# Performance work log

Hardware: AMD Instinct MI355X
Metric: run time of the kernel (lower is better)

## Reference

```python
import jax, jax.numpy as jnp
import numpy as np

B, T, D = 2, 4096, 1024
H, L = 8, 2
DH = D // H           # 128
BS = 64               # bucket_size (lucidrains default)
NH = 8                # n_hashes (lucidrains default)
NB = T // BS          # 64 buckets (even, required)
FF = 4 * D


def setup_inputs() -> dict:
    key = jax.random.key(0)
    ks = jax.random.split(key, 16)
    s = 0.02
    return {
        'x': jax.random.normal(ks[0], (B, T, D), jnp.float32),
        'Wqk': jax.random.normal(ks[1], (L, D, H * DH), jnp.float32) * s,
        'Wv': jax.random.normal(ks[2], (L, D, H * DH), jnp.float32) * s,
        'Wout': jax.random.normal(ks[3], (L, H * DH, D), jnp.float32) * s,
        'bout': jnp.zeros((L, D), jnp.float32),
        'ln1_g': jnp.ones((L, D), jnp.float32),
        'ln1_b': jnp.zeros((L, D), jnp.float32),
        'W1': jax.random.normal(ks[4], (L, D, FF), jnp.float32) * s,
        'b1': jnp.zeros((L, FF), jnp.float32),
        'W2': jax.random.normal(ks[5], (L, FF, D), jnp.float32) * s,
        'b2': jnp.zeros((L, D), jnp.float32),
        'ln2_g': jnp.ones((L, D), jnp.float32),
        'ln2_b': jnp.zeros((L, D), jnp.float32),
        'rotations': jax.random.normal(ks[6], (L, DH, NH, NB // 2), jnp.float32),
    }


def _layer_norm(x, g, b):
    m = jnp.mean(x, axis=-1, keepdims=True)
    v = jnp.var(x, axis=-1, keepdims=True)
    return (x - m) * jax.lax.rsqrt(v + 1e-5) * g + b


def _look_one_back(x):
    # concat each chunk with the previous chunk (wrap-around), along the within-chunk axis
    return jnp.concatenate([x, jnp.roll(x, 1, axis=1)], axis=2)


def _lsh_attention(qk, v, rot):
    # qk, v: (bh, T, DH); rot: (DH, NH, NB//2). Causal LSH attention (lucidrains defaults).
    bh, t, d = qk.shape
    rotated = jnp.einsum('btd,dhr->bhtr', qk, rot)
    rotated = jnp.concatenate([rotated, -rotated], axis=-1)          # (bh, NH, T, NB)
    buckets = jnp.argmax(rotated, axis=-1)                            # (bh, NH, T)
    buckets = buckets + (jnp.arange(NH) * NB)[None, :, None]
    buckets = buckets.reshape(bh, NH * t)
    ticker = jnp.arange(NH * t)
    buckets_and_t = buckets * t + (ticker % t)
    sticker = jnp.argsort(buckets_and_t, axis=-1)                     # stable
    undo_sort = jnp.argsort(sticker, axis=-1)
    st = sticker % t                                                  # original positions
    sqk = jnp.take_along_axis(qk, st[..., None], axis=1)              # (bh, NH*T, DH)
    sv = jnp.take_along_axis(v, st[..., None], axis=1)
    n_chunks = NH * NB
    bq = sqk.reshape(bh, n_chunks, BS, d)
    norm = jnp.maximum(jnp.linalg.norm(sqk, axis=-1, keepdims=True), 1e-12)
    bk = (sqk / norm).reshape(bh, n_chunks, BS, d)
    bv = sv.reshape(bh, n_chunks, BS, d)
    bk = _look_one_back(bk)                                           # (bh, nc, 2*BS, d)
    bv = _look_one_back(bv)
    dots = jnp.einsum('bcie,bcje->bcij', bq, bk) * (d ** -0.5)
    bq_t = st.reshape(bh, n_chunks, BS)
    bkv_t = _look_one_back(bq_t[..., None] * jnp.ones((1,), st.dtype))[..., 0] if False else jnp.concatenate([bq_t, jnp.roll(bq_t, 1, axis=1)], axis=2)
    causal = bq_t[:, :, :, None] < bkv_t[:, :, None, :]
    dots = jnp.where(causal, -1e9, dots)
    self_mask = bq_t[:, :, :, None] == bkv_t[:, :, None, :]
    dots = jnp.where(self_mask, -5e4, dots)                           # TOKEN_SELF_ATTN_VALUE
    lse = jax.scipy.special.logsumexp(dots, axis=-1, keepdims=True)
    p = jnp.exp(dots - lse)
    bo = jnp.einsum('bcij,bcje->bcie', p, bv)
    so = bo.reshape(bh, NH * t, d)
    o = jnp.take_along_axis(so, undo_sort[..., None], axis=1)
    logits = jnp.take_along_axis(lse.reshape(bh, NH * t), undo_sort, axis=1)
    o = o.reshape(bh, NH, t, d)
    logits = logits.reshape(bh, NH, t, 1)
    probs = jnp.exp(logits - jax.scipy.special.logsumexp(logits, axis=1, keepdims=True))
    return jnp.sum(o * probs, axis=1)                                 # (bh, T, DH)


def _attn_block(x, Wqk, Wv, Wout, bout, g, b, rot):
    h = _layer_norm(x, g, b)
    qk = (h @ Wqk).reshape(B, T, H, DH).transpose(0, 2, 1, 3).reshape(B * H, T, DH)
    v = (h @ Wv).reshape(B, T, H, DH).transpose(0, 2, 1, 3).reshape(B * H, T, DH)
    o = _lsh_attention(qk, v, rot)
    o = o.reshape(B, H, T, DH).transpose(0, 2, 1, 3).reshape(B, T, H * DH)
    return o @ Wout + bout


def _ff_block(x, W1, b1, W2, b2, g, b):
    h = _layer_norm(x, g, b)
    return jax.nn.gelu(h @ W1 + b1, approximate=False) @ W2 + b2


def reference(x, Wqk, Wv, Wout, bout, ln1_g, ln1_b, W1, b1, W2, b2, ln2_g, ln2_b, rotations):
    # Reversible Reformer: x duplicated into two streams
    x1, x2 = x, x
    for l in range(L):
        x1 = x1 + _attn_block(x2, Wqk[l], Wv[l], Wout[l], bout[l], ln1_g[l], ln1_b[l], rotations[l])
        x2 = x2 + _ff_block(x1, W1[l], b1[l], W2[l], b2[l], ln2_g[l], ln2_b[l])
    out = (x1 + x2) * 0.5
    # mean-pool over sequence, reshape (1, B, D)
    return jnp.mean(out, axis=1).reshape(1, -1, D)
```

## Files before the change

### kernel.cpp

```cpp
#include <hip/hip_runtime.h>
#include <hip/hip_bf16.h>
#include <stdint.h>

#define B_ 2
#define T_ 4096
#define D_ 1024
#define H_ 8
#define DH_ 128
#define L_ 2
#define BS_ 64
#define NH_ 8
#define NB_ 64
#define NC_ (NH_*NB_)
#define FF_ 4096
#define BH_ (B_*H_)

typedef __hip_bfloat16 bf16;
typedef __attribute__((ext_vector_type(8))) short short8;
typedef __attribute__((ext_vector_type(4))) float f32x4;

typedef __attribute__((address_space(3))) uint32_t lds_u32_t;
typedef const __attribute__((address_space(1))) uint32_t glb_u32_t;

__device__ __forceinline__ void async_load16(const void* g, void* l) {
  __builtin_amdgcn_global_load_lds((glb_u32_t*)g, (lds_u32_t*)l, 16, 0, 0);
}

__global__ void diag_kernel(float* __restrict__ out, float a, float b) {
  if (threadIdx.x == 0) { out[0] = a; out[1] = b; }
}

__global__ void copy2_kernel(const float* __restrict__ x, float* __restrict__ x1,
                             float* __restrict__ x2) {
  int idx = blockIdx.x * 256 + threadIdx.x;
  if (idx < B_ * T_ * D_ / 4) {
    float4 v = ((const float4*)x)[idx];
    ((float4*)x1)[idx] = v;
    ((float4*)x2)[idx] = v;
  }
}

__global__ __launch_bounds__(256)
void transpose_cvt(const float* __restrict__ src, bf16* __restrict__ dst, int K, int N) {
  __shared__ float tile[32][33];
  const int n0 = blockIdx.x * 32, k0 = blockIdx.y * 32;
  const int c = threadIdx.x & 31, r8 = threadIdx.x >> 5;
#pragma unroll
  for (int i = 0; i < 32; i += 8) tile[r8 + i][c] = src[(size_t)(k0 + r8 + i) * N + n0 + c];
  __syncthreads();
#pragma unroll
  for (int i = 0; i < 32; i += 8)
    dst[(size_t)(n0 + r8 + i) * K + k0 + c] = __float2bfloat16(tile[c][r8 + i]);
}

__global__ __launch_bounds__(256)
void ln_kernel(const float* __restrict__ x, const float* __restrict__ g,
               const float* __restrict__ b, bf16* __restrict__ h) {
  __shared__ float red[8];
  const int row = blockIdx.x;
  const float* xr = x + (size_t)row * D_;
  const int tid = threadIdx.x;
  float4 xv = *(const float4*)(xr + tid * 4);
  float vals[4] = {xv.x, xv.y, xv.z, xv.w};
  float s = vals[0] + vals[1] + vals[2] + vals[3];
  float s2 = vals[0]*vals[0] + vals[1]*vals[1] + vals[2]*vals[2] + vals[3]*vals[3];
#pragma unroll
  for (int o = 1; o < 64; o <<= 1) { s += __shfl_xor(s, o, 64); s2 += __shfl_xor(s2, o, 64); }
  const int w = tid >> 6, lane = tid & 63;
  if (lane == 0) { red[w] = s; red[4 + w] = s2; }
  __syncthreads();
  s = red[0] + red[1] + red[2] + red[3];
  s2 = red[4] + red[5] + red[6] + red[7];
  const float mean = s * (1.0f / D_);
  const float var = s2 * (1.0f / D_) - mean * mean;
  const float rstd = rsqrtf(var + 1e-5f);
  bf16* hr = h + (size_t)row * D_;
#pragma unroll
  for (int i = 0; i < 4; ++i) {
    const int c = tid * 4 + i;
    hr[c] = __float2bfloat16((vals[i] - mean) * rstd * g[c] + b[c]);
  }
}

template<int EPI>
__global__ __launch_bounds__(512)
void gemm256(const bf16* __restrict__ A, const bf16* __restrict__ Bt,
             void* __restrict__ dst, const float* __restrict__ bias,
             float* __restrict__ resid, int M, int N, int K) {
  __shared__ __align__(16) bf16 sA[2][256 * 64];
  __shared__ __align__(16) bf16 sB[2][256 * 64];
  const int tid = threadIdx.x;

  const int GX = gridDim.x;
  const int nwg = GX * gridDim.y;
  const int orig = blockIdx.y * GX + blockIdx.x;
  int m0, n0;
  if ((nwg & 7) == 0 && (gridDim.y & 7) == 0) {
    const int cpx = nwg >> 3;
    const int lin = (orig & 7) * cpx + (orig >> 3);
    const int gsz = GX << 3;
    const int group = lin / gsz;
    const int rem = lin - group * gsz;
    m0 = ((group << 3) + (rem & 7)) << 8;
    n0 = (rem >> 3) << 8;
  } else {
    m0 = blockIdx.y << 8;
    n0 = blockIdx.x << 8;
  }

  const int lane = tid & 63;
  const int wv = tid >> 6;
  const int wm = (wv >> 2) << 7;
  const int wn = (wv & 3) << 6;
  const int l15 = lane & 15, lq = lane >> 4;

  f32x4 acc[8][4];
#pragma unroll
  for (int i = 0; i < 8; ++i)
#pragma unroll
    for (int j = 0; j < 4; ++j) acc[i][j] = (f32x4){0.f, 0.f, 0.f, 0.f};

  const bf16* Ab = A + (size_t)m0 * K;
  const bf16* Bb = Bt + (size_t)n0 * K;
  const int ch0 = tid & 7;

  auto stage_pass = [&](int buf, int t, int p) {
    const size_t ko = (size_t)t << 6;
    const int r = (tid >> 3) + (p << 6);
    const size_t ga = (size_t)r * K + (size_t)((ch0 ^ (r & 7)) << 3) + ko;
    async_load16(Ab + ga, (char*)sA[buf] + (p << 13) + tid * 16);
    async_load16(Bb + ga, (char*)sB[buf] + (p << 13) + tid * 16);
  };

#pragma unroll
  for (int p = 0; p < 4; ++p) stage_pass(0, 0, p);
  __syncthreads();

  const int NT = K >> 6;
  short8 bfr[4][2];
  for (int t = 0; t < NT; ++t) {
    const int cur = t & 1;
    const bf16* __restrict__ pA = sA[cur];
    const bf16* __restrict__ pB = sB[cur];
#pragma unroll
    for (int p = 0; p < 4; ++p) {
      if (t + 1 < NT) stage_pass(cur ^ 1, t + 1, p);
      if (p == 0) {
#pragma unroll
        for (int ni = 0; ni < 4; ++ni)
#pragma unroll
          for (int kk = 0; kk < 2; ++kk) {
            const int row = wn + ni * 16 + l15;
            bfr[ni][kk] = *(const short8*)(pB + (row << 6) + (((kk * 4 + lq) ^ (row & 7)) << 3));
          }
      }
      short8 af[2][2];
#pragma unroll
      for (int m2 = 0; m2 < 2; ++m2)
#pragma unroll
        for (int kk = 0; kk < 2; ++kk) {
          const int row = wm + (2 * p + m2) * 16 + l15;
          af[m2][kk] = *(const short8*)(pA + (row << 6) + (((kk * 4 + lq) ^ (row & 7)) << 3));
        }
      __builtin_amdgcn_s_setprio(1);
#pragma unroll
      for (int m2 = 0; m2 < 2; ++m2)
#pragma unroll
        for (int ni = 0; ni < 4; ++ni)
#pragma unroll
          for (int kk = 0; kk < 2; ++kk)
            acc[2 * p + m2][ni] =
                __builtin_amdgcn_mfma_f32_16x16x32_bf16(af[m2][kk], bfr[ni][kk], acc[2 * p + m2][ni], 0, 0, 0);
      __builtin_amdgcn_s_setprio(0);
    }
    if (t + 1 < NT) __syncthreads();
  }

  const int cr = lq << 2;
#pragma unroll
  for (int mi = 0; mi < 8; ++mi) {
#pragma unroll
    for (int ni = 0; ni < 4; ++ni) {
#pragma unroll
      for (int j = 0; j < 4; ++j) {
        const int r = m0 + wm + mi * 16 + cr + j;
        const int c = n0 + wn + ni * 16 + l15;
        const float val = acc[mi][ni][j];
        if (EPI == 0) {
          const int bb = r >> 12, t2 = r & (T_ - 1);
          if (c < 1024) {
            const int hh = c >> 7, dh = c & (DH_ - 1);
            ((bf16*)dst)[(((size_t)(bb * H_ + hh)) * T_ + t2) * DH_ + dh] = __float2bfloat16(val);
          } else {
            const int c2 = c - 1024;
            const int hh = c2 >> 7, dh = c2 & (DH_ - 1);
            ((bf16*)resid)[(((size_t)(bb * H_ + hh)) * T_ + t2) * DH_ + dh] = __float2bfloat16(val);
          }
        } else if (EPI == 3) {
          const float xg = val + bias[c];
          ((bf16*)dst)[(size_t)r * N + c] =
              __float2bfloat16(0.5f * xg * (1.0f + erff(xg * 0.70710678118654752440f)));
        }
      }
    }
  }
}

template<int EPI>
__global__ __launch_bounds__(512)
void gemm_bt_k(const bf16* __restrict__ A, const bf16* __restrict__ Bt,
               void* __restrict__ dst, const float* __restrict__ bias,
               float* __restrict__ resid, int M, int N, int K) {
  __shared__ __align__(16) bf16 sA[2][128 * 64];
  __shared__ __align__(16) bf16 sB[2][128 * 64];
  const int tid = threadIdx.x;

  const int GX = gridDim.x;
  const int nwg = GX * gridDim.y;
  const int orig = blockIdx.y * GX + blockIdx.x;
  int m0, n0;
  if ((nwg & 7) == 0 && (gridDim.y & 7) == 0) {
    const int cpx = nwg >> 3;
    const int lin = (orig & 7) * cpx + (orig >> 3);
    const int gsz = GX << 3;
    const int group = lin / gsz;
    const int rem = lin - group * gsz;
    m0 = ((group << 3) + (rem & 7)) << 7;
    n0 = (rem >> 3) << 7;
  } else {
    m0 = blockIdx.y << 7;
    n0 = blockIdx.x << 7;
  }

  const int lane = tid & 63;
  const int wv = tid >> 6;
  const int wm = (wv >> 2) << 6;
  const int wn = (wv & 3) << 5;
  const int l15 = lane & 15, lq = lane >> 4;

  f32x4 acc[4][2];
#pragma unroll
  for (int i = 0; i < 4; ++i)
#pragma unroll
    for (int j = 0; j < 2; ++j) acc[i][j] = (f32x4){0.f, 0.f, 0.f, 0.f};

  const bf16* Ab = A + (size_t)m0 * K;
  const bf16* Bb = Bt + (size_t)n0 * K;

  const int r0s = tid >> 3, ch0 = tid & 7;
  const int r1s = r0s + 64;
  const size_t sa0 = (size_t)r0s * K + (size_t)((ch0 ^ (r0s & 7)) << 3);
  const size_t sa1 = (size_t)r1s * K + (size_t)((ch0 ^ (r1s & 7)) << 3);

  auto stage = [&](int t) {
    const int b = t & 1;
    const size_t ko = (size_t)t << 6;
    async_load16(Ab + sa0 + ko, (char*)sA[b] + tid * 16);
    async_load16(Ab + sa1 + ko, (char*)sA[b] + (tid + 512) * 16);
    async_load16(Bb + sa0 + ko, (char*)sB[b] + tid * 16);
    async_load16(Bb + sa1 + ko, (char*)sB[b] + (tid + 512) * 16);
  };

  auto compute = [&](int b) {
    const bf16* __restrict__ pA = sA[b];
    const bf16* __restrict__ pB = sB[b];
#pragma unroll
    for (int kk = 0; kk < 2; ++kk) {
      short8 af[4], bfr[2];
#pragma unroll
      for (int mi = 0; mi < 4; ++mi) {
        const int row = wm + mi * 16 + l15;
        const int chunk = (kk * 4 + lq) ^ (row & 7);
        af[mi] = *(const short8*)(pA + (row << 6) + (chunk << 3));
      }
#pragma unroll
      for (int ni = 0; ni < 2; ++ni) {
        const int row = wn + ni * 16 + l15;
        const int chunk = (kk * 4 + lq) ^ (row & 7);
        bfr[ni] = *(const short8*)(pB + (row << 6) + (chunk << 3));
      }
#pragma unroll
      for (int mi = 0; mi < 4; ++mi)
#pragma unroll
        for (int ni = 0; ni < 2; ++ni)
          acc[mi][ni] = __builtin_amdgcn_mfma_f32_16x16x32_bf16(af[mi], bfr[ni], acc[mi][ni], 0, 0, 0);
    }
  };

  stage(0);
  __syncthreads();
  const int NT = K >> 6;
  for (int t = 0; t < NT; ++t) {
    if (t + 1 < NT) stage(t + 1);
    compute(t & 1);
    if (t + 1 < NT) __syncthreads();
  }

  const int cr = lq << 2;
  if (EPI == 5) {
    const int hh2 = (n0 + wn) >> 5;
#pragma unroll
    for (int mi = 0; mi < 4; ++mi) {
#pragma unroll
      for (int j = 0; j < 4; ++j) {
        const float v0 = acc[mi][0][j], v1 = acc[mi][1][j];
        float bmx = v0; int imx = l15;
        if (v1 > bmx) { bmx = v1; imx = 16 + l15; }
        float bmn = v0; int imn = l15;
        if (v1 < bmn) { bmn = v1; imn = 16 + l15; }
#pragma unroll
        for (int o = 1; o < 16; o <<= 1) {
          const float ov = __shfl_xor(bmx, o, 64); const int oi = __shfl_xor(imx, o, 64);
          if (ov > bmx || (ov == bmx && oi < imx)) { bmx = ov; imx = oi; }
          const float ov2 = __shfl_xor(bmn, o, 64); const int oi2 = __shfl_xor(imn, o, 64);
          if (ov2 < bmn || (ov2 == bmn && oi2 < imn)) { bmn = ov2; imn = oi2; }
        }
        if (l15 == 0) {
          const int r = m0 + wm + mi * 16 + cr + j;
          const int bh = r >> 12, t2 = r & (T_ - 1);
          const int bkt = (bmx >= -bmn) ? imx : 32 + imn;
          ((uint8_t*)dst)[((size_t)(bh * 8 + hh2) << 12) + t2] = (uint8_t)bkt;
        }
      }
    }
    return;
  }

#pragma unroll
  for (int mi = 0; mi < 4; ++mi) {
#pragma unroll
    for (int ni = 0; ni < 2; ++ni) {
#pragma unroll
      for (int j = 0; j < 4; ++j) {
        const int r = m0 + wm + mi * 16 + cr + j;
        const int c = n0 + wn + ni * 16 + l15;
        float val = acc[mi][ni][j];
        if (EPI == 0) {
          const int bb = r >> 12, t2 = r & (T_ - 1);
          const int hh = c >> 7, dh = c & (DH_ - 1);
          ((bf16*)dst)[(((size_t)(bb * H_ + hh)) * T_ + t2) * DH_ + dh] = __float2bfloat16(val);
        } else if (EPI == 2) {
          resid[(size_t)r * N + c] += val + bias[c];
        } else if (EPI == 3) {
          const float xg = val + bias[c];
          ((bf16*)dst)[(size_t)r * N + c] =
              __float2bfloat16(0.5f * xg * (1.0f + erff(xg * 0.70710678118654752440f)));
        } else if (EPI == 4) {
          ((bf16*)dst)[(size_t)r * N + c] = __float2bfloat16(val);
        }
      }
    }
  }
}

__global__ void bucket_kernel(const bf16* __restrict__ rotv, uint8_t* __restrict__ buckets) {
  const int idx = blockIdx.x * 256 + threadIdx.x;
  if (idx >= BH_ * T_ * NH_) return;
  const int row = idx >> 3, hh = idx & 7;
  const bf16* p = rotv + (size_t)row * 256 + hh * 32;
  float vmax = -3e38f, vmin = 3e38f;
  int imax = 0, imin = 0;
  for (int r = 0; r < 32; ++r) {
    const float xv = __bfloat162float(p[r]);
    if (xv > vmax) { vmax = xv; imax = r; }
    if (xv < vmin) { vmin = xv; imin = r; }
  }
  const int bkt = (vmax >= -vmin) ? imax : 32 + imin;
  const int bh = row >> 12, t = row & (T_ - 1);
  buckets[((size_t)(bh * 8 + hh) << 12) + t] = (uint8_t)bkt;
}

__global__ __launch_bounds__(256)
void sort_kernel(const uint8_t* __restrict__ buckets, int* __restrict__ st,
                 int* __restrict__ inv) {
  __shared__ uint8_t bk[T_];
  __shared__ int wsum[4];
  const int tid = threadIdx.x;
  const int grp = blockIdx.x;
  const uint8_t* src = buckets + (size_t)grp * T_;
  int* dst = st + (size_t)grp * T_;
  int* ivd = inv ? inv + (size_t)grp * T_ : nullptr;
  for (int i = tid; i < T_; i += 256) bk[i] = src[i];
  __syncthreads();
  const int lane = tid & 63, w = tid >> 6;
  const int t0 = tid * 16;
  int base = 0;
  for (int b = 0; b < 64; ++b) {
    int cnt = 0;
#pragma unroll
    for (int j = 0; j < 16; ++j) cnt += (bk[t0 + j] == b) ? 1 : 0;
    int incl = cnt;
    for (int o = 1; o < 64; o <<= 1) {
      int vv = __shfl_up(incl, o, 64);
      if (lane >= o) incl += vv;
    }
    if (lane == 63) wsum[w] = incl;
    __syncthreads();
    int wo = 0;
    for (int i = 0; i < w; ++i) wo += wsum[i];
    const int tot = wsum[0] + wsum[1] + wsum[2] + wsum[3];
    int pos = base + wo + incl - cnt;
    for (int j = 0; j < 16; ++j)
      if (bk[t0 + j] == b) {
        dst[pos] = t0 + j;
        if (ivd) ivd[t0 + j] = pos;
        ++pos;
      }
    base += tot;
    __syncthreads();
  }
}

__global__ __launch_bounds__(256)
void qknorm_kernel(const bf16* __restrict__ qk, bf16* __restrict__ qkn,
                   float* __restrict__ qnorm) {
  const int wid = (blockIdx.x * 256 + threadIdx.x) >> 6;
  const int lane = threadIdx.x & 63;
  if (wid >= BH_ * T_) return;
  const bf16* src = qk + (size_t)wid * DH_;
  const float a = __bfloat162float(src[2 * lane]);
  const float b = __bfloat162float(src[2 * lane + 1]);
  float ss = a * a + b * b;
#pragma unroll
  for (int o = 1; o < 64; o <<= 1) ss += __shfl_xor(ss, o, 64);
  const float nrm = sqrtf(ss);
  const float sc = 1.0f / fmaxf(nrm, 1e-12f);
  bf16* d = qkn + (size_t)wid * DH_;
  d[2 * lane] = __float2bfloat16(a * sc);
  d[2 * lane + 1] = __float2bfloat16(b * sc);
  if (lane == 0) qnorm[wid] = nrm;
}

__global__ __launch_bounds__(256)
void attn_sorted(const bf16* __restrict__ qkn, const float* __restrict__ qnormg,
                 const bf16* __restrict__ v, const int* __restrict__ st,
                 bf16* __restrict__ so, float* __restrict__ lseg) {
  __shared__ __align__(16) bf16 sK[128 * 136];
  __shared__ __align__(16) uint32_t sVT[128][68];
  __shared__ int stkv[128];
  __shared__ float snq[64];

  const int tid = threadIdx.x;
  const int lin = blockIdx.x;
  const int xcd = lin & 7;
  const int wq = lin >> 3;
  const int bh = xcd + ((wq >> 9) << 3);
  const int rem = wq & 511;
  const int hh = rem >> 6;
  const int cb = rem & 63;

  const int cg = hh * NB_ + cb;
  const int pg = (cg + NC_ - 1) & (NC_ - 1);
  const int* stb = st + (size_t)bh * (NH_ * T_);
  if (tid < 128) {
    const int p = (tid < 64) ? (cg * BS_ + tid) : (pg * BS_ + tid - 64);
    stkv[tid] = stb[p];
  }
  __syncthreads();

  const size_t vbase = (size_t)bh * T_ * DH_;
  if (tid < 64) snq[tid] = qnormg[(size_t)bh * T_ + stkv[tid]];
  {
    const int part = tid & 15, row = tid >> 4;
    for (int r0 = 0; r0 < 128; r0 += 16) {
      const int rr = r0 + row;
      const int t = stkv[rr];
      *(float4*)&sK[rr * 136 + part * 8] = *(const float4*)(qkn + vbase + (size_t)t * DH_ + part * 8);
    }
  }
  {
    for (int it = 0; it < 4; ++it) {
      const int idx = it * 256 + tid;
      const int g = idx & 15, kp = idx >> 4;
      const int t0 = stkv[2 * kp], t1 = stkv[2 * kp + 1];
      float4 a = *(const float4*)(v + vbase + (size_t)t0 * DH_ + g * 8);
      float4 b = *(const float4*)(v + vbase + (size_t)t1 * DH_ + g * 8);
      const unsigned short* ua = (const unsigned short*)&a;
      const unsigned short* ub = (const unsigned short*)&b;
      const int csw = (g & 7) << 2;
#pragma unroll
      for (int j = 0; j < 8; ++j)
        sVT[g * 8 + j][kp ^ csw] = (uint32_t)ua[j] | ((uint32_t)ub[j] << 16);
    }
  }
  __syncthreads();

  const int lane = tid & 63;
  const int w = tid >> 6;
  const int l15 = lane & 15, lq = lane >> 4;

  f32x4 acc[8];
#pragma unroll
  for (int i = 0; i < 8; ++i) acc[i] = (f32x4){0.f, 0.f, 0.f, 0.f};
#pragma unroll
  for (int kk = 0; kk < 4; ++kk) {
    short8 af = *(const short8*)&sK[(w * 16 + l15) * 136 + lq * 8 + kk * 32];
#pragma unroll
    for (int ni = 0; ni < 8; ++ni) {
      short8 bf = *(const short8*)&sK[(ni * 16 + l15) * 136 + lq * 8 + kk * 32];
      acc[ni] = __builtin_amdgcn_mfma_f32_16x16x32_bf16(af, bf, acc[ni], 0, 0, 0);
    }
  }
  __syncthreads();

  bf16* sP = sK;

  float lsev[4];
  const float scale = 0.08838834764831845f;
#pragma unroll
  for (int j = 0; j < 4; ++j) {
    const int row = w * 16 + lq * 4 + j;
    const int tq = stkv[row];
    const float rowsc = scale * snq[row];
    float mx = -3.0e38f;
#pragma unroll
    for (int ni = 0; ni < 8; ++ni) {
      const int tk = stkv[ni * 16 + l15];
      float val = acc[ni][j] * rowsc;
      if (tq < tk) val = -1e9f;
      else if (tq == tk) val = -5e4f;
      acc[ni][j] = val;
      mx = fmaxf(mx, val);
    }
#pragma unroll
    for (int o = 1; o < 16; o <<= 1) mx = fmaxf(mx, __shfl_xor(mx, o, 64));
    float ex[8];
    float se = 0.f;
#pragma unroll
    for (int ni = 0; ni < 8; ++ni) { ex[ni] = __expf(acc[ni][j] - mx); se += ex[ni]; }
#pragma unroll
    for (int o = 1; o < 16; o <<= 1) se += __shfl_xor(se, o, 64);
    const float inv = 1.0f / se;
#pragma unroll
    for (int ni = 0; ni < 8; ++ni)
      sP[row * 136 + ni * 16 + l15] = __float2bfloat16(ex[ni] * inv);
    lsev[j] = mx + __logf(se);
  }
  __syncthreads();

  f32x4 acc2[8];
#pragma unroll
  for (int i = 0; i < 8; ++i) acc2[i] = (f32x4){0.f, 0.f, 0.f, 0.f};
#pragma unroll
  for (int kk = 0; kk < 4; ++kk) {
    short8 pa = *(const short8*)&sP[(w * 16 + l15) * 136 + lq * 8 + kk * 32];
#pragma unroll
    for (int ni = 0; ni < 8; ++ni) {
      const int row = ni * 16 + l15;
      const int col = (lq * 4 + kk * 16) ^ (((row >> 3) & 7) << 2);
      short8 bv = *(const short8*)&sVT[row][col];
      acc2[ni] = __builtin_amdgcn_mfma_f32_16x16x32_bf16(pa, bv, acc2[ni], 0, 0, 0);
    }
  }

  const size_t sobase = ((size_t)(hh * BH_ + bh) * T_ + (size_t)cb * BS_) * DH_;
#pragma unroll
  for (int j = 0; j < 4; ++j) {
    const int row = w * 16 + lq * 4 + j;
    if (l15 == 0)
      lseg[(size_t)(hh * BH_ + bh) * T_ + cb * BS_ + row] = lsev[j];
    bf16* orow = so + sobase + (size_t)row * DH_;
#pragma unroll
    for (int ni = 0; ni < 8; ++ni) {
      bf16 hv = __float2bfloat16(acc2[ni][j]);
      __builtin_nontemporal_store(*(unsigned short*)&hv,
                                  (unsigned short*)(orow + ni * 16 + l15));
    }
  }
}

__global__ __launch_bounds__(256)
void combine2_kernel(const bf16* __restrict__ so, const float* __restrict__ lseg,
                     const int* __restrict__ ipos, bf16* __restrict__ ocomb) {
  const int gw = (blockIdx.x * 256 + threadIdx.x) >> 6;
  const int lane = threadIdx.x & 63;
  if (gw >= BH_ * T_) return;
  const int bh = gw >> 12, t = gw & (T_ - 1);
  float lse8 = -3.0e38f;
  int p8 = 0;
  if (lane < 8) {
    p8 = ipos[((size_t)bh * NH_ + lane) * T_ + t];
    lse8 = lseg[((size_t)lane * BH_ + bh) * T_ + p8];
  }
  float m = -3.0e38f;
#pragma unroll
  for (int h = 0; h < 8; ++h) m = fmaxf(m, __shfl(lse8, h, 64));
  float s = 0.f;
#pragma unroll
  for (int h = 0; h < 8; ++h) s += __expf(__shfl(lse8, h, 64) - m);
  const float invs = 1.0f / s;
  float a0 = 0.f, a1 = 0.f;
#pragma unroll
  for (int h = 0; h < 8; ++h) {
    const int ph = __shfl(p8, h, 64);
    const float wh = __expf(__shfl(lse8, h, 64) - m) * invs;
    const unsigned short* rp =
        (const unsigned short*)(so + (((size_t)h * BH_ + bh) * T_ + ph) * DH_ + lane * 2);
    unsigned short u0 = __builtin_nontemporal_load(rp);
    unsigned short u1 = __builtin_nontemporal_load(rp + 1);
    a0 += wh * __bfloat162float(*(const bf16*)&u0);
    a1 += wh * __bfloat162float(*(const bf16*)&u1);
  }
  const int bb = bh >> 3, hd = bh & 7;
  bf16* dp = ocomb + ((size_t)(bb * T_ + t)) * D_ + hd * DH_ + lane * 2;
  dp[0] = __float2bfloat16(a0);
  dp[1] = __float2bfloat16(a1);
}

__global__ __launch_bounds__(256)
void attn_kernel(const bf16* __restrict__ qkn, const float* __restrict__ qnormg,
                 const bf16* __restrict__ v, const int* __restrict__ st,
                 float* __restrict__ mg, float* __restrict__ sg,
                 float* __restrict__ oac, int hh) {
  __shared__ __align__(16) bf16 sK[128 * 136];
  __shared__ __align__(16) uint32_t sVT[128][68];
  __shared__ int stkv[128];
  __shared__ float snq[64];

  const int tid = threadIdx.x;
  const int cb = blockIdx.x;
  const int bh = blockIdx.y;
  const int cg = hh * NB_ + cb;
  const int pg = (cg + NC_ - 1) & (NC_ - 1);
  const int* stb = st + (size_t)bh * (NH_ * T_);
  if (tid < 128) {
    const int p = (tid < 64) ? (cg * BS_ + tid) : (pg * BS_ + tid - 64);
    stkv[tid] = stb[p];
  }
  __syncthreads();

  const size_t vbase = (size_t)bh * T_ * DH_;
  if (tid < 64) snq[tid] = qnormg[(size_t)bh * T_ + stkv[tid]];
  {
    const int part = tid & 15, row = tid >> 4;
    for (int r0 = 0; r0 < 128; r0 += 16) {
      const int rr = r0 + row;
      const int t = stkv[rr];
      *(float4*)&sK[rr * 136 + part * 8] = *(const float4*)(qkn + vbase + (size_t)t * DH_ + part * 8);
    }
  }
  {
    for (int it = 0; it < 4; ++it) {
      const int idx = it * 256 + tid;
      const int g = idx & 15, kp = idx >> 4;
      const int t0 = stkv[2 * kp], t1 = stkv[2 * kp + 1];
      float4 a = *(const float4*)(v + vbase + (size_t)t0 * DH_ + g * 8);
      float4 b = *(const float4*)(v + vbase + (size_t)t1 * DH_ + g * 8);
      const unsigned short* ua = (const unsigned short*)&a;
      const unsigned short* ub = (const unsigned short*)&b;
#pragma unroll
      for (int j = 0; j < 8; ++j)
        sVT[g * 8 + j][kp] = (uint32_t)ua[j] | ((uint32_t)ub[j] << 16);
    }
  }
  __syncthreads();

  const int lane = tid & 63;
  const int w = tid >> 6;
  const int l15 = lane & 15, lq = lane >> 4;

  f32x4 acc[8];
#pragma unroll
  for (int i = 0; i < 8; ++i) acc[i] = (f32x4){0.f, 0.f, 0.f, 0.f};
#pragma unroll
  for (int kk = 0; kk < 4; ++kk) {
    short8 af = *(const short8*)&sK[(w * 16 + l15) * 136 + lq * 8 + kk * 32];
#pragma unroll
    for (int ni = 0; ni < 8; ++ni) {
      short8 bf = *(const short8*)&sK[(ni * 16 + l15) * 136 + lq * 8 + kk * 32];
      acc[ni] = __builtin_amdgcn_mfma_f32_16x16x32_bf16(af, bf, acc[ni], 0, 0, 0);
    }
  }
  __syncthreads();

  bf16* sP = sK;

  float lsev[4];
  const float scale = 0.08838834764831845f;
#pragma unroll
  for (int j = 0; j < 4; ++j) {
    const int row = w * 16 + lq * 4 + j;
    const int tq = stkv[row];
    const float rowsc = scale * snq[row];
    float mx = -3.0e38f;
#pragma unroll
    for (int ni = 0; ni < 8; ++ni) {
      const int tk = stkv[ni * 16 + l15];
      float val = acc[ni][j] * rowsc;
      if (tq < tk) val = -1e9f;
      else if (tq == tk) val = -5e4f;
      acc[ni][j] = val;
      mx = fmaxf(mx, val);
    }
#pragma unroll
    for (int o = 1; o < 16; o <<= 1) mx = fmaxf(mx, __shfl_xor(mx, o, 64));
    float se = 0.f;
#pragma unroll
    for (int ni = 0; ni < 8; ++ni) se += __expf(acc[ni][j] - mx);
#pragma unroll
    for (int o = 1; o < 16; o <<= 1) se += __shfl_xor(se, o, 64);
    const float inv = 1.0f / se;
#pragma unroll
    for (int ni = 0; ni < 8; ++ni)
      sP[row * 136 + ni * 16 + l15] = __float2bfloat16(__expf(acc[ni][j] - mx) * inv);
    lsev[j] = mx + __logf(se);
  }
  __syncthreads();

  f32x4 acc2[8];
#pragma unroll
  for (int i = 0; i < 8; ++i) acc2[i] = (f32x4){0.f, 0.f, 0.f, 0.f};
#pragma unroll
  for (int kk = 0; kk < 4; ++kk) {
    short8 pa = *(const short8*)&sP[(w * 16 + l15) * 136 + lq * 8 + kk * 32];
#pragma unroll
    for (int ni = 0; ni < 8; ++ni) {
      short8 bv = *(const short8*)&sVT[ni * 16 + l15][lq * 4 + kk * 16];
      acc2[ni] = __builtin_amdgcn_mfma_f32_16x16x32_bf16(pa, bv, acc2[ni], 0, 0, 0);
    }
  }

#pragma unroll
  for (int j = 0; j < 4; ++j) {
    const int row = w * 16 + lq * 4 + j;
    const int t = stkv[row];
    const size_t gi = (size_t)bh * T_ + t;
    const float ls = lsev[j];
    float* orow = oac + gi * DH_;
    if (hh == 0) {
      if (l15 == 0) { sg[gi] = 1.0f; mg[gi] = ls; }
#pragma unroll
      for (int ni = 0; ni < 8; ++ni) orow[ni * 16 + l15] = acc2[ni][j];
    } else {
      const float mo = mg[gi];
      const float mn = fmaxf(mo, ls);
      const float al = __expf(mo - mn);
      const float be = __expf(ls - mn);
      if (l15 == 0) { sg[gi] = sg[gi] * al + be; mg[gi] = mn; }
#pragma unroll
      for (int ni = 0; ni < 8; ++ni) {
        const int c = ni * 16 + l15;
        orow[c] = orow[c] * al + be * acc2[ni][j];
      }
    }
  }
}

__global__ void combine_kernel(const float* __restrict__ oac, const float* __restrict__ sg,
                               bf16* __restrict__ ocomb) {
  const int idx = blockIdx.x * 256 + threadIdx.x;
  if (idx >= BH_ * T_ * DH_ / 4) return;
  const int rowtok = idx >> 5;
  const int gsub = idx & 31;
  const float inv = 1.0f / sg[rowtok];
  float4 ov = ((const float4*)oac)[idx];
  const int bh = rowtok >> 12, t = rowtok & (T_ - 1);
  const int bb = bh >> 3, hd = bh & 7;
  bf16* dp = ocomb + ((size_t)(bb * T_ + t)) * D_ + hd * DH_ + gsub * 4;
  dp[0] = __float2bfloat16(ov.x * inv);
  dp[1] = __float2bfloat16(ov.y * inv);
  dp[2] = __float2bfloat16(ov.z * inv);
  dp[3] = __float2bfloat16(ov.w * inv);
}

__global__ void pool_partial(const float* __restrict__ x1, const float* __restrict__ x2,
                             float* __restrict__ part) {
  const int b = blockIdx.y, slice = blockIdx.x;
  const int tid = threadIdx.x;
  float acc[4] = {0.f, 0.f, 0.f, 0.f};
  for (int r = 0; r < 32; ++r) {
    const size_t base = ((size_t)b * T_ + slice * 32 + r) * D_;
#pragma unroll
    for (int i = 0; i < 4; ++i) {
      const int c = tid + i * 256;
      acc[i] += x1[base + c] + x2[base + c];
    }
  }
#pragma unroll
  for (int i = 0; i < 4; ++i)
    part[((size_t)(b * 128 + slice)) * D_ + tid + i * 256] = acc[i];
}

__global__ void pool_reduce(const float* __restrict__ part, float* __restrict__ out) {
  const int idx = blockIdx.x * 256 + threadIdx.x;
  if (idx >= B_ * D_) return;
  const int b = idx >> 10, d = idx & 1023;
  float s = 0.f;
  for (int k = 0; k < 128; ++k) s += part[((size_t)(b * 128 + k)) * D_ + d];
  out[idx] = s * (0.5f / T_);
}

extern "C" void kernel_launch(void* const* d_in, const int* in_sizes, int n_in,
                              void* d_out, int out_size, void* d_ws, size_t ws_size,
                              hipStream_t stream) {
  (void)in_sizes; (void)n_in; (void)out_size;
  const float* x    = (const float*)d_in[0];
  const float* Wqk  = (const float*)d_in[1];
  const float* Wv   = (const float*)d_in[2];
  const float* Wout = (const float*)d_in[3];
  const float* bout = (const float*)d_in[4];
  const float* ln1g = (const float*)d_in[5];
  const float* ln1b = (const float*)d_in[6];
  const float* W1   = (const float*)d_in[7];
  const float* b1   = (const float*)d_in[8];
  const float* W2   = (const float*)d_in[9];
  const float* b2   = (const float*)d_in[10];
  const float* ln2g = (const float*)d_in[11];
  const float* ln2b = (const float*)d_in[12];
  const float* rot  = (const float*)d_in[13];
  float* out = (float*)d_out;

  char* ws = (char*)d_ws;
  const dim3 blk(256);
  const dim3 blk512(512);

  {
    size_t off = 0;
    auto alloc = [&](size_t b) { size_t o = off; off += (b + 255) & ~(size_t)255; return o; };
    const size_t o_x1  = alloc((size_t)B_ * T_ * D_ * 4);
    const size_t o_x2  = alloc((size_t)B_ * T_ * D_ * 4);
    const size_t o_hq  = alloc((size_t)B_ * T_ * D_ * 2);
    const size_t o_qk  = alloc((size_t)BH_ * T_ * DH_ * 2);
    const size_t o_vv  = alloc((size_t)BH_ * T_ * DH_ * 2);
    const size_t o_so  = alloc((size_t)NH_ * BH_ * T_ * DH_ * 2);
    const size_t o_lse = alloc((size_t)NH_ * BH_ * T_ * 4);
    const size_t o_st  = alloc((size_t)BH_ * NH_ * T_ * 4);
    const size_t o_ip  = alloc((size_t)BH_ * NH_ * T_ * 4);
    const size_t o_bkt = alloc((size_t)BH_ * NH_ * T_);
    const size_t o_qn  = alloc((size_t)BH_ * T_ * 4);
    const size_t o_part = alloc((size_t)B_ * 128 * D_ * 4);

    if (off <= ws_size) {
      float* x1   = (float*)(ws + o_x1);
      float* x2   = (float*)(ws + o_x2);
      bf16*  h    = (bf16*)(ws + o_hq);
      bf16*  qkn  = (bf16*)(ws + o_hq);
      bf16*  qk   = (bf16*)(ws + o_qk);
      bf16*  ocomb = (bf16*)(ws + o_qk);
      bf16*  vv   = (bf16*)(ws + o_vv);
      bf16*  so   = (bf16*)(ws + o_so);
      float* lse  = (float*)(ws + o_lse);
      int*   st   = (int*)(ws + o_st);
      int*   ip   = (int*)(ws + o_ip);
      uint8_t* bkt = (uint8_t*)(ws + o_bkt);
      float* qn   = (float*)(ws + o_qn);
      float* part = (float*)(ws + o_part);
      bf16* wqkT = (bf16*)(ws + o_so);
      bf16* wvT  = wqkT + (size_t)D_ * D_;
      bf16* rotT = wvT + (size_t)D_ * D_;
      bf16* woT  = (bf16*)(ws + o_so);
      bf16* ffh  = (bf16*)(ws + o_so);
      bf16* w1T  = (bf16*)(ws + o_so + ((size_t)64 << 20));
      bf16* w2T  = w1T + (size_t)D_ * FF_;

      copy2_kernel<<<dim3(B_ * T_ * D_ / 4 / 256), blk, 0, stream>>>(x, x1, x2);

      for (int l = 0; l < L_; ++l) {
        transpose_cvt<<<dim3(32, 32), blk, 0, stream>>>(Wqk + (size_t)l * D_ * D_, wqkT, D_, D_);
        transpose_cvt<<<dim3(32, 32), blk, 0, stream>>>(Wv + (size_t)l * D_ * D_, wvT, D_, D_);
        transpose_cvt<<<dim3(8, 4), blk, 0, stream>>>(rot + (size_t)l * DH_ * 256, rotT, DH_, 256);

        ln_kernel<<<dim3(B_ * T_), blk, 0, stream>>>(x2, ln1g + l * D_, ln1b + l * D_, h);
        gemm256<0><<<dim3(8, 32), blk512, 0, stream>>>(h, wqkT, qk, nullptr, (float*)vv,
                                                       B_ * T_, 2048, D_);
        qknorm_kernel<<<dim3(BH_ * T_ / 4), blk, 0, stream>>>(qk, qkn, qn);
        gemm_bt_k<5><<<dim3(2, 512), blk512, 0, stream>>>(qkn, rotT, bkt, nullptr, nullptr, BH_ * T_, 256, DH_);
        sort_kernel<<<dim3(BH_ * NH_), blk, 0, stream>>>(bkt, st, ip);
        attn_sorted<<<dim3(NB_ * BH_ * NH_), blk, 0, stream>>>(qkn, qn, vv, st, so, lse);
        combine2_kernel<<<dim3(BH_ * T_ / 4), blk, 0, stream>>>(so, lse, ip, ocomb);
        transpose_cvt<<<dim3(32, 32), blk, 0, stream>>>(Wout + (size_t)l * D_ * D_, woT, D_, D_);
        gemm_bt_k<2><<<dim3(8, 64), blk512, 0, stream>>>(ocomb, woT, nullptr, bout + l * D_, x1, B_ * T_, D_, D_);

        transpose_cvt<<<dim3(128, 32), blk, 0, stream>>>(W1 + (size_t)l * D_ * FF_, w1T, D_, FF_);
        transpose_cvt<<<dim3(32, 128), blk, 0, stream>>>(W2 + (size_t)l * FF_ * D_, w2T, FF_, D_);
        ln_kernel<<<dim3(B_ * T_), blk, 0, stream>>>(x1, ln2g + l * D_, ln2b + l * D_, h);
        gemm256<3><<<dim3(16, 32), blk512, 0, stream>>>(h, w1T, ffh, b1 + l * FF_,
                                                        nullptr, B_ * T_, FF_, D_);
        gemm_bt_k<2><<<dim3(8, 64), blk512, 0, stream>>>(ffh, w2T, nullptr, b2 + l * D_, x2, B_ * T_, D_, FF_);
      }

      pool_partial<<<dim3(128, B_), blk, 0, stream>>>(x1, x2, part);
      pool_reduce<<<dim3((B_ * D_ + 255) / 256), blk, 0, stream>>>(part, out);
      return;
    }
  }

  size_t off = 0;
  auto alloc = [&](size_t b) { size_t o = off; off += (b + 255) & ~(size_t)255; return o; };
  const size_t o_x1   = alloc((size_t)B_ * T_ * D_ * 4);
  const size_t o_x2   = alloc((size_t)B_ * T_ * D_ * 4);
  const size_t o_hq   = alloc((size_t)B_ * T_ * D_ * 2);
  const size_t o_qk   = alloc((size_t)BH_ * T_ * DH_ * 2);
  const size_t o_vv   = alloc((size_t)BH_ * T_ * DH_ * 2);
  const size_t o_oac  = alloc((size_t)BH_ * T_ * DH_ * 4);
  const size_t o_st   = alloc((size_t)BH_ * NH_ * T_ * 4);
  const size_t o_bkt  = alloc((size_t)BH_ * NH_ * T_);
  const size_t o_mg   = alloc((size_t)BH_ * T_ * 4);
  const size_t o_sg   = alloc((size_t)BH_ * T_ * 4);
  const size_t o_qn   = alloc((size_t)BH_ * T_ * 4);
  const size_t o_part = alloc((size_t)B_ * 128 * D_ * 4);
  const size_t o_w    = alloc((size_t)D_ * FF_ * 2 * 2);
  if (off > ws_size) {
    diag_kernel<<<dim3(1), dim3(64), 0, stream>>>(out, (float)ws_size, (float)off);
    return;
  }

  float* x1   = (float*)(ws + o_x1);
  float* x2   = (float*)(ws + o_x2);
  bf16*  h    = (bf16*)(ws + o_hq);
  bf16*  qkn  = (bf16*)(ws + o_hq);
  bf16*  qk   = (bf16*)(ws + o_qk);
  bf16*  ocomb = (bf16*)(ws + o_qk);
  bf16*  vv   = (bf16*)(ws + o_vv);
  float* oac  = (float*)(ws + o_oac);
  bf16*  rotd = (bf16*)(ws + o_oac);
  bf16*  ffh  = (bf16*)(ws + o_qk);
  int*   st   = (int*)(ws + o_st);
  uint8_t* bkt = (uint8_t*)(ws + o_bkt);
  float* mg   = (float*)(ws + o_mg);
  float* sg   = (float*)(ws + o_sg);
  float* qn   = (float*)(ws + o_qn);
  float* part = (float*)(ws + o_part);
  bf16* wqkT = (bf16*)(ws + o_w);
  bf16* wvT  = (bf16*)(ws + o_w + (size_t)D_ * D_ * 2);
  bf16* woT  = (bf16*)(ws + o_w + (size_t)D_ * D_ * 2 * 2);
  bf16* rotT = (bf16*)(ws + o_w + (size_t)D_ * D_ * 2 * 3);
  bf16* w1T  = (bf16*)(ws + o_w);
  bf16* w2T  = (bf16*)(ws + o_w + (size_t)D_ * FF_ * 2);

  copy2_kernel<<<dim3(B_ * T_ * D_ / 4 / 256), blk, 0, stream>>>(x, x1, x2);

  for (int l = 0; l < L_; ++l) {
    transpose_cvt<<<dim3(32, 32), blk, 0, stream>>>(Wqk + (size_t)l * D_ * D_, wqkT, D_, D_);
    transpose_cvt<<<dim3(32, 32), blk, 0, stream>>>(Wv + (size_t)l * D_ * D_, wvT, D_, D_);
    transpose_cvt<<<dim3(32, 32), blk, 0, stream>>>(Wout + (size_t)l * D_ * D_, woT, D_, D_);
    transpose_cvt<<<dim3(8, 4), blk, 0, stream>>>(rot + (size_t)l * DH_ * 256, rotT, DH_, 256);

    ln_kernel<<<dim3(B_ * T_), blk, 0, stream>>>(x2, ln1g + l * D_, ln1b + l * D_, h);
    gemm_bt_k<0><<<dim3(8, 64), blk512, 0, stream>>>(h, wqkT, qk, nullptr, nullptr, B_ * T_, D_, D_);
    gemm_bt_k<0><<<dim3(8, 64), blk512, 0, stream>>>(h, wvT, vv, nullptr, nullptr, B_ * T_, D_, D_);
    qknorm_kernel<<<dim3(BH_ * T_ / 4), blk, 0, stream>>>(qk, qkn, qn);
    gemm_bt_k<4><<<dim3(2, 512), blk512, 0, stream>>>(qkn, rotT, rotd, nullptr, nullptr, BH_ * T_, 256, DH_);
    bucket_kernel<<<dim3(BH_ * T_ * NH_ / 256), blk, 0, stream>>>(rotd, bkt);
    sort_kernel<<<dim3(BH_ * NH_), blk, 0, stream>>>(bkt, st, nullptr);
    for (int hh = 0; hh < NH_; ++hh)
      attn_kernel<<<dim3(NB_, BH_), blk, 0, stream>>>(qkn, qn, vv, st, mg, sg, oac, hh);
    combine_kernel<<<dim3(BH_ * T_ * DH_ / 4 / 256), blk, 0, stream>>>(oac, sg, ocomb);
    gemm_bt_k<2><<<dim3(8, 64), blk512, 0, stream>>>(ocomb, woT, nullptr, bout + l * D_, x1, B_ * T_, D_, D_);

    transpose_cvt<<<dim3(128, 32), blk, 0, stream>>>(W1 + (size_t)l * D_ * FF_, w1T, D_, FF_);
    transpose_cvt<<<dim3(32, 128), blk, 0, stream>>>(W2 + (size_t)l * FF_ * D_, w2T, FF_, D_);

    ln_kernel<<<dim3(B_ * T_), blk, 0, stream>>>(x1, ln2g + l * D_, ln2b + l * D_, h);
    gemm_bt_k<3><<<dim3(32, 64), blk512, 0, stream>>>(h, w1T, ffh, b1 + l * FF_, nullptr, B_ * T_, FF_, D_);
    gemm_bt_k<2><<<dim3(8, 64), blk512, 0, stream>>>(ffh, w2T, nullptr, b2 + l * D_, x2, B_ * T_, D_, FF_);
  }

  pool_partial<<<dim3(128, B_), blk, 0, stream>>>(x1, x2, part);
  pool_reduce<<<dim3((B_ * D_ + 255) / 256), blk, 0, stream>>>(part, out);
}
```

Measured before the change: 1.196 ms.

## Pipeline 256-tile GEMM with split-phase async loads and reduce attention LDS footprint

The 256x256 GEMM main loop is restructured so B-tile prefetches are issued in two halves and A-tile prefetches after a mid-iteration barrier. Explicit vmcnt waits replace the full __syncthreads, which lets a single shared-memory buffer pair be refilled while MFMAs still run on the current data. In the sorted LSH attention kernel, V rows are loaded into registers early and written transposed to LDS only after the softmax. Half of the transposed V buffer reuses the freed K region, which cuts LDS use and may allow more resident workgroups, at the cost of extra registers and tricky wait-count correctness.

New measurement: 1.123 ms. -6.1%, faster.

```diff
diff --git a/kernel.cpp b/kernel.cpp
--- a/kernel.cpp
+++ b/kernel.cpp
@@ -84,9 +84,9 @@
 
 template<int EPI>
 __global__ __launch_bounds__(512)
-void gemm256(const bf16* __restrict__ A, const bf16* __restrict__ Bt,
-             void* __restrict__ dst, const float* __restrict__ bias,
-             float* __restrict__ resid, int M, int N, int K) {
+void gemm256p(const bf16* __restrict__ A, const bf16* __restrict__ Bt,
+              void* __restrict__ dst, const float* __restrict__ bias,
+              float* __restrict__ resid, int M, int N, int K) {
   __shared__ __align__(16) bf16 sA[2][256 * 64];
   __shared__ __align__(16) bf16 sB[2][256 * 64];
   const int tid = threadIdx.x;
@@ -122,58 +122,116 @@
 
   const bf16* Ab = A + (size_t)m0 * K;
   const bf16* Bb = Bt + (size_t)n0 * K;
-  const int ch0 = tid & 7;
-
-  auto stage_pass = [&](int buf, int t, int p) {
-    const size_t ko = (size_t)t << 6;
-    const int r = (tid >> 3) + (p << 6);
-    const size_t ga = (size_t)r * K + (size_t)((ch0 ^ (r & 7)) << 3) + ko;
-    async_load16(Ab + ga, (char*)sA[buf] + (p << 13) + tid * 16);
-    async_load16(Bb + ga, (char*)sB[buf] + (p << 13) + tid * 16);
+  const int rs = tid >> 3, ch0 = tid & 7;
+
+  auto stageA = [&](int t, int q) {
+    const int r = (q << 6) + rs;
+    const size_t ga = (size_t)r * K + (size_t)((ch0 ^ (r & 7)) << 3) + ((size_t)t << 6);
+    async_load16(Ab + ga, (char*)sA[t & 1] + (q << 13) + tid * 16);
   };
-
-#pragma unroll
-  for (int p = 0; p < 4; ++p) stage_pass(0, 0, p);
-  __syncthreads();
+  auto stageB = [&](int t, int q) {
+    const int r = (q << 6) + rs;
+    const size_t ga = (size_t)r * K + (size_t)((ch0 ^ (r & 7)) << 3) + ((size_t)t << 6);
+    async_load16(Bb + ga, (char*)sB[t & 1] + (q << 13) + tid * 16);
+  };
+
+  short8 bfr[4][2];
+
+#pragma unroll
+  for (int q = 0; q < 4; ++q) { stageB(0, q); stageA(0, q); }
+  asm volatile("s_waitcnt vmcnt(0)" ::: "memory");
+  __builtin_amdgcn_s_barrier();
 
   const int NT = K >> 6;
-  short8 bfr[4][2];
   for (int t = 0; t < NT; ++t) {
-    const int cur = t & 1;
-    const bf16* __restrict__ pA = sA[cur];
-    const bf16* __restrict__ pB = sB[cur];
-#pragma unroll
-    for (int p = 0; p < 4; ++p) {
-      if (t + 1 < NT) stage_pass(cur ^ 1, t + 1, p);
-      if (p == 0) {
-#pragma unroll
-        for (int ni = 0; ni < 4; ++ni)
-#pragma unroll
-          for (int kk = 0; kk < 2; ++kk) {
-            const int row = wn + ni * 16 + l15;
-            bfr[ni][kk] = *(const short8*)(pB + (row << 6) + (((kk * 4 + lq) ^ (row & 7)) << 3));
-          }
+    const int b = t & 1;
+    const bool more = (t + 1 < NT);
+    const bf16* __restrict__ pA = sA[b];
+    const bf16* __restrict__ pB = sB[b];
+
+    if (more) { stageB(t + 1, 0); stageB(t + 1, 1); }
+#pragma unroll
+    for (int ni = 0; ni < 4; ++ni)
+#pragma unroll
+      for (int kk = 0; kk < 2; ++kk) {
+        const int row = wn + ni * 16 + l15;
+        bfr[ni][kk] = *(const short8*)(pB + (row << 6) + (((kk * 4 + lq) ^ (row & 7)) << 3));
       }
-      short8 af[2][2];
-#pragma unroll
-      for (int m2 = 0; m2 < 2; ++m2)
-#pragma unroll
-        for (int kk = 0; kk < 2; ++kk) {
-          const int row = wm + (2 * p + m2) * 16 + l15;
-          af[m2][kk] = *(const short8*)(pA + (row << 6) + (((kk * 4 + lq) ^ (row & 7)) << 3));
-        }
+#pragma unroll
+    for (int m2 = 0; m2 < 2; ++m2) {
+      short8 af[2];
+      const int row = wm + m2 * 16 + l15;
+#pragma unroll
+      for (int kk = 0; kk < 2; ++kk)
+        af[kk] = *(const short8*)(pA + (row << 6) + (((kk * 4 + lq) ^ (row & 7)) << 3));
       __builtin_amdgcn_s_setprio(1);
 #pragma unroll
-      for (int m2 = 0; m2 < 2; ++m2)
-#pragma unroll
-        for (int ni = 0; ni < 4; ++ni)
-#pragma unroll
-          for (int kk = 0; kk < 2; ++kk)
-            acc[2 * p + m2][ni] =
-                __builtin_amdgcn_mfma_f32_16x16x32_bf16(af[m2][kk], bfr[ni][kk], acc[2 * p + m2][ni], 0, 0, 0);
+      for (int ni = 0; ni < 4; ++ni)
+#pragma unroll
+        for (int kk = 0; kk < 2; ++kk)
+          acc[m2][ni] = __builtin_amdgcn_mfma_f32_16x16x32_bf16(af[kk], bfr[ni][kk], acc[m2][ni], 0, 0, 0);
       __builtin_amdgcn_s_setprio(0);
     }
-    if (t + 1 < NT) __syncthreads();
+
+    if (more) { stageB(t + 1, 2); stageB(t + 1, 3); }
+#pragma unroll
+    for (int m2 = 0; m2 < 2; ++m2) {
+      short8 af[2];
+      const int row = wm + (2 + m2) * 16 + l15;
+#pragma unroll
+      for (int kk = 0; kk < 2; ++kk)
+        af[kk] = *(const short8*)(pA + (row << 6) + (((kk * 4 + lq) ^ (row & 7)) << 3));
+      __builtin_amdgcn_s_setprio(1);
+#pragma unroll
+      for (int ni = 0; ni < 4; ++ni)
+#pragma unroll
+        for (int kk = 0; kk < 2; ++kk)
+          acc[2 + m2][ni] = __builtin_amdgcn_mfma_f32_16x16x32_bf16(af[kk], bfr[ni][kk], acc[2 + m2][ni], 0, 0, 0);
+      __builtin_amdgcn_s_setprio(0);
+    }
+
+    if (more) asm volatile("s_waitcnt vmcnt(4)" ::: "memory");
+    else      asm volatile("s_waitcnt vmcnt(0)" ::: "memory");
+    __builtin_amdgcn_s_barrier();
+
+    if (more) { stageA(t + 1, 0); stageA(t + 1, 2); }
+#pragma unroll
+    for (int m2 = 0; m2 < 2; ++m2) {
+      short8 af[2];
+      const int row = wm + (4 + m2) * 16 + l15;
+#pragma unroll
+      for (int kk = 0; kk < 2; ++kk)
+        af[kk] = *(const short8*)(pA + (row << 6) + (((kk * 4 + lq) ^ (row & 7)) << 3));
+      __builtin_amdgcn_s_setprio(1);
+#pragma unroll
+      for (int ni = 0; ni < 4; ++ni)
+#pragma unroll
+        for (int kk = 0; kk < 2; ++kk)
+          acc[4 + m2][ni] = __builtin_amdgcn_mfma_f32_16x16x32_bf16(af[kk], bfr[ni][kk], acc[4 + m2][ni], 0, 0, 0);
+      __builtin_amdgcn_s_setprio(0);
+    }
+
+    if (more) { stageA(t + 1, 1); stageA(t + 1, 3); }
+#pragma unroll
+    for (int m2 = 0; m2 < 2; ++m2) {
+      short8 af[2];
+      const int row = wm + (6 + m2) * 16 + l15;
+#pragma unroll
+      for (int kk = 0; kk < 2; ++kk)
+        af[kk] = *(const short8*)(pA + (row << 6) + (((kk * 4 + lq) ^ (row & 7)) << 3));
+      __builtin_amdgcn_s_setprio(1);
+#pragma unroll
+      for (int ni = 0; ni < 4; ++ni)
+#pragma unroll
+        for (int kk = 0; kk < 2; ++kk)
+          acc[6 + m2][ni] = __builtin_amdgcn_mfma_f32_16x16x32_bf16(af[kk], bfr[ni][kk], acc[6 + m2][ni], 0, 0, 0);
+      __builtin_amdgcn_s_setprio(0);
+    }
+
+    if (more) {
+      asm volatile("s_waitcnt vmcnt(2)" ::: "memory");
+      __builtin_amdgcn_s_barrier();
+    }
   }
 
   const int cr = lq << 2;
@@ -186,7 +244,11 @@
         const int r = m0 + wm + mi * 16 + cr + j;
         const int c = n0 + wn + ni * 16 + l15;
         const float val = acc[mi][ni][j];
-        if (EPI == 0) {
+        if (EPI == 3) {
+          const float xg = val + bias[c];
+          ((bf16*)dst)[(size_t)r * N + c] =
+              __float2bfloat16(0.5f * xg * (1.0f + erff(xg * 0.70710678118654752440f)));
+        } else if (EPI == 6) {
           const int bb = r >> 12, t2 = r & (T_ - 1);
           if (c < 1024) {
             const int hh = c >> 7, dh = c & (DH_ - 1);
@@ -196,10 +258,6 @@
             const int hh = c2 >> 7, dh = c2 & (DH_ - 1);
             ((bf16*)resid)[(((size_t)(bb * H_ + hh)) * T_ + t2) * DH_ + dh] = __float2bfloat16(val);
           }
-        } else if (EPI == 3) {
-          const float xg = val + bias[c];
-          ((bf16*)dst)[(size_t)r * N + c] =
-              __float2bfloat16(0.5f * xg * (1.0f + erff(xg * 0.70710678118654752440f)));
         }
       }
     }
@@ -347,6 +405,16 @@
               __float2bfloat16(0.5f * xg * (1.0f + erff(xg * 0.70710678118654752440f)));
         } else if (EPI == 4) {
           ((bf16*)dst)[(size_t)r * N + c] = __float2bfloat16(val);
+        } else if (EPI == 6) {
+          const int bb = r >> 12, t2 = r & (T_ - 1);
+          if (c < 1024) {
+            const int hh = c >> 7, dh = c & (DH_ - 1);
+            ((bf16*)dst)[(((size_t)(bb * H_ + hh)) * T_ + t2) * DH_ + dh] = __float2bfloat16(val);
+          } else {
+            const int c2 = c - 1024;
+            const int hh = c2 >> 7, dh = c2 & (DH_ - 1);
+            ((bf16*)resid)[(((size_t)(bb * H_ + hh)) * T_ + t2) * DH_ + dh] = __float2bfloat16(val);
+          }
         }
       }
     }
@@ -436,7 +504,7 @@
                  const bf16* __restrict__ v, const int* __restrict__ st,
                  bf16* __restrict__ so, float* __restrict__ lseg) {
   __shared__ __align__(16) bf16 sK[128 * 136];
-  __shared__ __align__(16) uint32_t sVT[128][68];
+  __shared__ __align__(16) uint32_t sVTlo[64 * 68];
   __shared__ int stkv[128];
   __shared__ float snq[64];
 
@@ -468,20 +536,13 @@
       *(float4*)&sK[rr * 136 + part * 8] = *(const float4*)(qkn + vbase + (size_t)t * DH_ + part * 8);
     }
   }
-  {
-    for (int it = 0; it < 4; ++it) {
-      const int idx = it * 256 + tid;
-      const int g = idx & 15, kp = idx >> 4;
-      const int t0 = stkv[2 * kp], t1 = stkv[2 * kp + 1];
-      float4 a = *(const float4*)(v + vbase + (size_t)t0 * DH_ + g * 8);
-      float4 b = *(const float4*)(v + vbase + (size_t)t1 * DH_ + g * 8);
-      const unsigned short* ua = (const unsigned short*)&a;
-      const unsigned short* ub = (const unsigned short*)&b;
-      const int csw = (g & 7) << 2;
-#pragma unroll
-      for (int j = 0; j < 8; ++j)
-        sVT[g * 8 + j][kp ^ csw] = (uint32_t)ua[j] | ((uint32_t)ub[j] << 16);
-    }
+  float4 va[4], vb[4];
+#pragma unroll
+  for (int it = 0; it < 4; ++it) {
+    const int idx = it * 256 + tid;
+    const int g = idx & 15, kp = idx >> 4;
+    va[it] = *(const float4*)(v + vbase + (size_t)stkv[2 * kp] * DH_ + g * 8);
+    vb[it] = *(const float4*)(v + vbase + (size_t)stkv[2 * kp + 1] * DH_ + g * 8);
   }
   __syncthreads();
 
@@ -504,6 +565,7 @@
   __syncthreads();
 
   bf16* sP = sK;
+  uint32_t* sVThi = (uint32_t*)(sK + 64 * 136);
 
   float lsev[4];
   const float scale = 0.08838834764831845f;
@@ -536,6 +598,19 @@
       sP[row * 136 + ni * 16 + l15] = __float2bfloat16(ex[ni] * inv);
     lsev[j] = mx + __logf(se);
   }
+
+#pragma unroll
+  for (int it = 0; it < 4; ++it) {
+    const int idx = it * 256 + tid;
+    const int g = idx & 15, kp = idx >> 4;
+    const unsigned short* ua = (const unsigned short*)&va[it];
+    const unsigned short* ub = (const unsigned short*)&vb[it];
+    const int csw = (g & 7) << 2;
+    uint32_t* vdst = (g < 8) ? (sVTlo + g * 8 * 68) : (sVThi + (g - 8) * 8 * 68);
+#pragma unroll
+    for (int j = 0; j < 8; ++j)
+      vdst[j * 68 + (kp ^ csw)] = (uint32_t)ua[j] | ((uint32_t)ub[j] << 16);
+  }
   __syncthreads();
 
   f32x4 acc2[8];
@@ -548,7 +623,8 @@
     for (int ni = 0; ni < 8; ++ni) {
       const int row = ni * 16 + l15;
       const int col = (lq * 4 + kk * 16) ^ (((row >> 3) & 7) << 2);
-      short8 bv = *(const short8*)&sVT[row][col];
+      const uint32_t* vrow = (ni < 4) ? (sVTlo + row * 68) : (sVThi + (row - 64) * 68);
+      short8 bv = *(const short8*)&vrow[col];
       acc2[ni] = __builtin_amdgcn_mfma_f32_16x16x32_bf16(pa, bv, acc2[ni], 0, 0, 0);
     }
   }
@@ -861,8 +937,8 @@
         transpose_cvt<<<dim3(8, 4), blk, 0, stream>>>(rot + (size_t)l * DH_ * 256, rotT, DH_, 256);
 
         ln_kernel<<<dim3(B_ * T_), blk, 0, stream>>>(x2, ln1g + l * D_, ln1b + l * D_, h);
-        gemm256<0><<<dim3(8, 32), blk512, 0, stream>>>(h, wqkT, qk, nullptr, (float*)vv,
-                                                       B_ * T_, 2048, D_);
+        gemm256p<6><<<dim3(8, 32), blk512, 0, stream>>>(h, wqkT, qk, nullptr, (float*)vv,
+                                                        B_ * T_, 2048, D_);
         qknorm_kernel<<<dim3(BH_ * T_ / 4), blk, 0, stream>>>(qk, qkn, qn);
         gemm_bt_k<5><<<dim3(2, 512), blk512, 0, stream>>>(qkn, rotT, bkt, nullptr, nullptr, BH_ * T_, 256, DH_);
         sort_kernel<<<dim3(BH_ * NH_), blk, 0, stream>>>(bkt, st, ip);
@@ -874,8 +950,8 @@
         transpose_cvt<<<dim3(128, 32), blk, 0, stream>>>(W1 + (size_t)l * D_ * FF_, w1T, D_, FF_);
         transpose_cvt<<<dim3(32, 128), blk, 0, stream>>>(W2 + (size_t)l * FF_ * D_, w2T, FF_, D_);
         ln_kernel<<<dim3(B_ * T_), blk, 0, stream>>>(x1, ln2g + l * D_, ln2b + l * D_, h);
-        gemm256<3><<<dim3(16, 32), blk512, 0, stream>>>(h, w1T, ffh, b1 + l * FF_,
-                                                        nullptr, B_ * T_, FF_, D_);
+        gemm256p<3><<<dim3(16, 32), blk512, 0, stream>>>(h, w1T, ffh, b1 + l * FF_,
+                                                         nullptr, B_ * T_, FF_, D_);
         gemm_bt_k<2><<<dim3(8, 64), blk512, 0, stream>>>(ffh, w2T, nullptr, b2 + l * D_, x2, B_ * T_, D_, FF_);
       }
 
```
